# Kernel optimization log

Measured on AMD Instinct MI355X. Metric: run time of the kernel, lower is better.

## Reference

```python
import jax, jax.numpy as jnp
import numpy as np

B, D, L, E, R = 16384, 512, 3, 4, 128

def setup_inputs() -> dict:
    key = jax.random.key(0)
    ks = jax.random.split(key, 6)
    scale = 0.05  # keep tanh in its non-saturated regime, like glorot-ish init
    return {
        "x":  jax.random.normal(ks[0], (B, D), dtype=jnp.float32),
        "Us": jax.random.normal(ks[1], (L, E, D, R), dtype=jnp.float32) * scale,
        "Cs": jax.random.normal(ks[2], (L, E, R, R), dtype=jnp.float32) * scale,
        "Vs": jax.random.normal(ks[3], (L, E, D, R), dtype=jnp.float32) * scale,
        "G":  jax.random.normal(ks[4], (L, E, D), dtype=jnp.float32) * scale,
        "b":  jnp.zeros((L, D), dtype=jnp.float32),
    }

def reference(x, Us, Cs, Vs, G, b):
    # x: (B, D). Original keeps x as (B, D, 1); we drop the trailing singleton.
    x0 = x
    xl = x
    num_layers = Us.shape[0]
    for i in range(num_layers):  # small fixed layer count
        U, C, V, g, bias = Us[i], Cs[i], Vs[i], G[i], b[i]
        # per-expert low-rank bilinear transform, fused over experts via einsum
        xv = jnp.tanh(jnp.einsum('edr,bd->ber', V, xl))       # (B, E, R)
        xc = jnp.tanh(jnp.einsum('ers,bes->ber', C, xv))      # (B, E, R)
        xu = jnp.einsum('edr,ber->bed', U, xc)                # (B, E, D)
        cross = x0[:, None, :] * (xu + bias[None, None, :])   # (B, E, D) experts
        # gating: Dense(1, no bias) per expert -> scores (B, E, 1)
        scores = jnp.einsum('bd,ed->be', xl, g)[..., None]
        # NOTE: original applies softmax over the LAST axis of (B, E, 1),
        # a singleton axis, so gates are all ones. Reproduced faithfully.
        gate = jax.nn.softmax(scores, axis=-1)                # (B, E, 1) of ones
        moe = jnp.einsum('bed,be->bd', cross, gate[..., 0])   # (B, D)
        xl = moe + xl
    return xl
```

## Files before the change

### kernel.cpp

```cpp
#include <hip/hip_runtime.h>
#include <hip/hip_bf16.h>

#define BATCH  16384
#define DIM    512
#define NLAYER 3
#define NEXP   4
#define RANK   128

typedef __bf16 bf16_t;
typedef bf16_t bf16x8 __attribute__((ext_vector_type(8)));
typedef bf16_t bf16x4 __attribute__((ext_vector_type(4)));
typedef float  f32x4  __attribute__((ext_vector_type(4)));

__device__ __forceinline__ float tanh_fast(float x) {
    float e = __expf(2.0f * x);
    return 1.0f - 2.0f * __builtin_amdgcn_rcpf(e + 1.0f);
}
__device__ __forceinline__ int swz(int row, int b) { return b ^ ((row & 7) << 4); }

__device__ __forceinline__ bf16x8 ldsr(const bf16_t* base, int row, int kb) {
    return *(const bf16x8*)((const char*)base + row * 1024 + swz(row, kb));
}
__device__ __forceinline__ void ldsw2(bf16_t* base, int row, int cb, bf16_t v) {
    *(bf16_t*)((char*)base + row * 1024 + swz(row, cb)) = v;
}
__device__ __forceinline__ void barrier_lds() {
    asm volatile("s_waitcnt lgkmcnt(0)" ::: "memory");
    __builtin_amdgcn_s_barrier();
}

__global__ void prep_pack(const float* __restrict__ Vs,
                          const float* __restrict__ Us,
                          const float* __restrict__ Cs,
                          bf16_t* __restrict__ Vp,
                          bf16_t* __restrict__ Up,
                          bf16_t* __restrict__ Cp) {
    int t = blockIdx.x * 256 + threadIdx.x;
    if (t < 98304) {
        int lane = t & 63, ni = (t >> 6) & 3, ks = (t >> 8) & 15,
            wn = (t >> 12) & 7, l = t >> 15;
        int c = wn * 64 + ni * 16 + (lane & 15), e = c >> 7, r = c & 127;
        int d0 = ks * 32 + (lane >> 4) * 8;
        const float* src = Vs + ((size_t)(l * NEXP + e) * DIM + d0) * RANK + r;
        bf16x8 v;
        #pragma unroll
        for (int j = 0; j < 8; ++j) v[j] = (bf16_t)src[j * RANK];
        *(bf16x8*)(Vp + (size_t)t * 8) = v;
    } else if (t < 196608) {
        int q = t - 98304;
        int lane = q & 63, ni = (q >> 6) & 3, ks = (q >> 8) & 15,
            wn = (q >> 12) & 7, l = q >> 15;
        int d = wn * 64 + ni * 16 + (lane & 15);
        int k0 = ks * 32 + (lane >> 4) * 8, e = k0 >> 7, r0 = k0 & 127;
        const float* src = Us + ((size_t)(l * NEXP + e) * DIM + d) * RANK + r0;
        bf16x8 v;
        #pragma unroll
        for (int j = 0; j < 8; ++j) v[j] = (bf16_t)src[j];
        *(bf16x8*)(Up + (size_t)q * 8) = v;
    } else if (t < 221184) {
        int q = t - 196608;
        int lane = q & 63, ni = (q >> 6) & 3, k4 = (q >> 8) & 3,
            wn = (q >> 10) & 7, l = q >> 13;
        int e = wn >> 1, rp = (wn & 1) * 64 + ni * 16 + (lane & 15);
        int s0 = k4 * 32 + (lane >> 4) * 8;
        const float* src = Cs + ((size_t)(l * NEXP + e) * RANK + rp) * RANK + s0;
        bf16x8 v;
        #pragma unroll
        for (int j = 0; j < 8; ++j) v[j] = (bf16_t)src[j];
        *(bf16x8*)(Cp + (size_t)q * 8) = v;
    }
}


__global__ __launch_bounds__(512)
void fused3(const float* __restrict__ x,
            const bf16_t* __restrict__ Vp,
            const bf16_t* __restrict__ Up,
            const bf16_t* __restrict__ Cp,
            const float* __restrict__ bb,
            float* __restrict__ out)
{
    __shared__ __align__(16) char smem[65536];
    bf16_t* bufA = (bf16_t*)smem;
    bf16_t* bufB = (bf16_t*)(smem + 32768);

    const int tid  = threadIdx.x;
    const int lane = tid & 63;
    const int wn   = tid >> 6;
    const int lr   = lane & 15;
    const int lg   = lane >> 4;
    const int m0   = blockIdx.x * 32;

    #pragma unroll
    for (int it = 0; it < 8; ++it) {
        int q = tid + 512 * it;
        int row = q >> 7, c4 = (q & 127) << 2;
        float4 v = *(const float4*)(x + (size_t)(m0 + row) * DIM + c4);
        bf16x4 b4 = { (bf16_t)v.x, (bf16_t)v.y, (bf16_t)v.z, (bf16_t)v.w };
        *(bf16x4*)((char*)bufA + row * 1024 + swz(row, c4 * 2)) = b4;
    }
    f32x4  xlf[2][4];
    bf16x4 x0r[2][4];
    #pragma unroll
    for (int mi = 0; mi < 2; ++mi)
        #pragma unroll
        for (int ni = 0; ni < 4; ++ni)
            #pragma unroll
            for (int j = 0; j < 4; ++j) {
                int row = mi * 16 + lg * 4 + j, col = wn * 64 + ni * 16 + lr;
                float v = x[(size_t)(m0 + row) * DIM + col];
                xlf[mi][ni][j] = v;
                x0r[mi][ni][j] = (bf16_t)v;
            }
    barrier_lds();

    #pragma unroll 1
    for (int l = 0; l < NLAYER; ++l) {
        bf16_t* xl_b = (l & 1) ? bufB : bufA;
        bf16_t* xv_b = (l & 1) ? bufA : bufB;

        const bf16_t* Vw = Vp + (((size_t)l * 8 + wn) << 15) + lane * 8;
        const bf16_t* Uw = Up + (((size_t)l * 8 + wn) << 15) + lane * 8;
        const bf16_t* Cw = Cp + (((size_t)l * 8 + wn) << 13) + lane * 8;

        {
            f32x4 a1[2][4] = {};
            const bf16_t* vp = Vw;
            #pragma unroll 8
            for (int ks = 0; ks < 16; ++ks) {
                bf16x8 bv[4];
                #pragma unroll
                for (int ni = 0; ni < 4; ++ni)
                    bv[ni] = *(const bf16x8*)(vp + ni * 512);
                vp += 2048;
                #pragma unroll
                for (int mi = 0; mi < 2; ++mi) {
                    bf16x8 av = ldsr(xl_b, mi * 16 + lr, ks * 64 + lg * 16);
                    #pragma unroll
                    for (int ni = 0; ni < 4; ++ni)
                        a1[mi][ni] = __builtin_amdgcn_mfma_f32_16x16x32_bf16(
                            av, bv[ni], a1[mi][ni], 0, 0, 0);
                }
            }
            #pragma unroll
            for (int mi = 0; mi < 2; ++mi)
                #pragma unroll
                for (int ni = 0; ni < 4; ++ni)
                    #pragma unroll
                    for (int j = 0; j < 4; ++j)
                        ldsw2(xv_b, mi * 16 + lg * 4 + j,
                              (wn * 64 + ni * 16 + lr) * 2,
                              (bf16_t)tanh_fast(a1[mi][ni][j]));
            barrier_lds();
        }

        {
            const int eb = (wn >> 1) * 256;
            f32x4 a2[2][4] = {};
            #pragma unroll
            for (int k4 = 0; k4 < 4; ++k4) {
                bf16x8 av[2];
                #pragma unroll
                for (int mi = 0; mi < 2; ++mi)
                    av[mi] = ldsr(xv_b, mi * 16 + lr, eb + k4 * 64 + lg * 16);
                #pragma unroll
                for (int ni = 0; ni < 4; ++ni) {
                    bf16x8 bv = *(const bf16x8*)(Cw + (k4 * 4 + ni) * 512);
                    #pragma unroll
                    for (int mi = 0; mi < 2; ++mi)
                        a2[mi][ni] = __builtin_amdgcn_mfma_f32_16x16x32_bf16(
                            av[mi], bv, a2[mi][ni], 0, 0, 0);
                }
            }
            #pragma unroll
            for (int mi = 0; mi < 2; ++mi)
                #pragma unroll
                for (int ni = 0; ni < 4; ++ni)
                    #pragma unroll
                    for (int j = 0; j < 4; ++j)
                        ldsw2(xl_b, mi * 16 + lg * 4 + j,
                              (wn * 64 + ni * 16 + lr) * 2,
                              (bf16_t)tanh_fast(a2[mi][ni][j]));
            barrier_lds();
        }

        {
            f32x4 a3[2][4] = {};
            const bf16_t* up = Uw;
            #pragma unroll 8
            for (int ks = 0; ks < 16; ++ks) {
                bf16x8 bv[4];
                #pragma unroll
                for (int ni = 0; ni < 4; ++ni)
                    bv[ni] = *(const bf16x8*)(up + ni * 512);
                up += 2048;
                #pragma unroll
                for (int mi = 0; mi < 2; ++mi) {
                    bf16x8 av = ldsr(xl_b, mi * 16 + lr, ks * 64 + lg * 16);
                    #pragma unroll
                    for (int ni = 0; ni < 4; ++ni)
                        a3[mi][ni] = __builtin_amdgcn_mfma_f32_16x16x32_bf16(
                            av, bv[ni], a3[mi][ni], 0, 0, 0);
                }
            }

            const float* bl = bb + l * DIM;
            #pragma unroll
            for (int ni = 0; ni < 4; ++ni) {
                int col = wn * 64 + ni * 16 + lr;
                float b4v = 4.0f * bl[col];
                #pragma unroll
                for (int mi = 0; mi < 2; ++mi)
                    #pragma unroll
                    for (int j = 0; j < 4; ++j)
                        xlf[mi][ni][j] +=
                            (float)x0r[mi][ni][j] * (a3[mi][ni][j] + b4v);
            }
        }

        if (l < NLAYER - 1) {
            #pragma unroll
            for (int mi = 0; mi < 2; ++mi)
                #pragma unroll
                for (int ni = 0; ni < 4; ++ni)
                    #pragma unroll
                    for (int j = 0; j < 4; ++j)
                        ldsw2(xv_b, mi * 16 + lg * 4 + j,
                              (wn * 64 + ni * 16 + lr) * 2,
                              (bf16_t)xlf[mi][ni][j]);
            barrier_lds();
        }
    }

    #pragma unroll
    for (int mi = 0; mi < 2; ++mi)
        #pragma unroll
        for (int ni = 0; ni < 4; ++ni)
            #pragma unroll
            for (int j = 0; j < 4; ++j) {
                int row = mi * 16 + lg * 4 + j, col = wn * 64 + ni * 16 + lr;
                out[(size_t)(m0 + row) * DIM + col] = xlf[mi][ni][j];
            }
}


extern "C" void kernel_launch(void* const* d_in, const int* in_sizes, int n_in,
                              void* d_out, int out_size, void* d_ws, size_t ws_size,
                              hipStream_t stream) {
    const float* x  = (const float*)d_in[0];
    const float* Us = (const float*)d_in[1];
    const float* Cs = (const float*)d_in[2];
    const float* Vs = (const float*)d_in[3];
    const float* bb = (const float*)d_in[5];
    float* out = (float*)d_out;

    bf16_t* Vp = (bf16_t*)d_ws;
    bf16_t* Up = Vp + 786432;
    bf16_t* Cp = Up + 786432;

    prep_pack<<<864, 256, 0, stream>>>(Vs, Us, Cs, Vp, Up, Cp);
    fused3<<<BATCH / 32, 512, 0, stream>>>(x, Vp, Up, Cp, bb, out);
}
```

Baseline: 123.4 us.

## Double batch rows per block and park residual state in AGPRs

Each block now handles 64 batch rows instead of 32, so every weight fragment loaded from global memory is reused across four 16-row MFMA tiles rather than two, halving weight traffic per row. The running fp32 residual is kept in accumulation registers through inline accvgpr read/write, freeing VGPRs for the larger accumulator tiles. The residual update is fused with the LDS write-back and the final output store. LDS use doubles to 128 KB, which allows one block per CU, and loop unrolling drops from 8 to 2 to limit register pressure, at some cost in latency hiding.

```diff
diff --git a/kernel.cpp b/kernel.cpp
--- a/kernel.cpp
+++ b/kernel.cpp
@@ -27,6 +27,14 @@
 __device__ __forceinline__ void barrier_lds() {
     asm volatile("s_waitcnt lgkmcnt(0)" ::: "memory");
     __builtin_amdgcn_s_barrier();
+}
+__device__ __forceinline__ void ag_w(float& a, float v) {
+    asm volatile("v_accvgpr_write_b32 %0, %1" : "=a"(a) : "v"(v));
+}
+__device__ __forceinline__ float ag_r(float a) {
+    float v;
+    asm volatile("v_accvgpr_read_b32 %0, %1" : "=v"(v) : "a"(a));
+    return v;
 }
 
 __global__ void prep_pack(const float* __restrict__ Vs,
@@ -80,36 +88,36 @@
             const float* __restrict__ bb,
             float* __restrict__ out)
 {
-    __shared__ __align__(16) char smem[65536];
+    __shared__ __align__(16) char smem[131072];
     bf16_t* bufA = (bf16_t*)smem;
-    bf16_t* bufB = (bf16_t*)(smem + 32768);
+    bf16_t* bufB = (bf16_t*)(smem + 65536);
 
     const int tid  = threadIdx.x;
     const int lane = tid & 63;
     const int wn   = tid >> 6;
     const int lr   = lane & 15;
     const int lg   = lane >> 4;
-    const int m0   = blockIdx.x * 32;
+    const int m0   = blockIdx.x * 64;
 
     #pragma unroll
-    for (int it = 0; it < 8; ++it) {
+    for (int it = 0; it < 16; ++it) {
         int q = tid + 512 * it;
         int row = q >> 7, c4 = (q & 127) << 2;
         float4 v = *(const float4*)(x + (size_t)(m0 + row) * DIM + c4);
         bf16x4 b4 = { (bf16_t)v.x, (bf16_t)v.y, (bf16_t)v.z, (bf16_t)v.w };
         *(bf16x4*)((char*)bufA + row * 1024 + swz(row, c4 * 2)) = b4;
     }
-    f32x4  xlf[2][4];
-    bf16x4 x0r[2][4];
+    float   xs[4][4][4];
+    bf16x4  x0r[4][4];
     #pragma unroll
-    for (int mi = 0; mi < 2; ++mi)
+    for (int mi = 0; mi < 4; ++mi)
         #pragma unroll
         for (int ni = 0; ni < 4; ++ni)
             #pragma unroll
             for (int j = 0; j < 4; ++j) {
                 int row = mi * 16 + lg * 4 + j, col = wn * 64 + ni * 16 + lr;
                 float v = x[(size_t)(m0 + row) * DIM + col];
-                xlf[mi][ni][j] = v;
+                ag_w(xs[mi][ni][j], v);
                 x0r[mi][ni][j] = (bf16_t)v;
             }
     barrier_lds();
@@ -124,9 +132,9 @@
         const bf16_t* Cw = Cp + (((size_t)l * 8 + wn) << 13) + lane * 8;
 
         {
-            f32x4 a1[2][4] = {};
+            f32x4 a1[4][4] = {};
             const bf16_t* vp = Vw;
-            #pragma unroll 8
+            #pragma unroll 2
             for (int ks = 0; ks < 16; ++ks) {
                 bf16x8 bv[4];
                 #pragma unroll
@@ -134,7 +142,7 @@
                     bv[ni] = *(const bf16x8*)(vp + ni * 512);
                 vp += 2048;
                 #pragma unroll
-                for (int mi = 0; mi < 2; ++mi) {
+                for (int mi = 0; mi < 4; ++mi) {
                     bf16x8 av = ldsr(xl_b, mi * 16 + lr, ks * 64 + lg * 16);
                     #pragma unroll
                     for (int ni = 0; ni < 4; ++ni)
@@ -143,7 +151,7 @@
                 }
             }
             #pragma unroll
-            for (int mi = 0; mi < 2; ++mi)
+            for (int mi = 0; mi < 4; ++mi)
                 #pragma unroll
                 for (int ni = 0; ni < 4; ++ni)
                     #pragma unroll
@@ -156,24 +164,24 @@
 
         {
             const int eb = (wn >> 1) * 256;
-            f32x4 a2[2][4] = {};
-            #pragma unroll
+            f32x4 a2[4][4] = {};
+            #pragma unroll 2
             for (int k4 = 0; k4 < 4; ++k4) {
-                bf16x8 av[2];
-                #pragma unroll
-                for (int mi = 0; mi < 2; ++mi)
-                    av[mi] = ldsr(xv_b, mi * 16 + lr, eb + k4 * 64 + lg * 16);
-                #pragma unroll
-                for (int ni = 0; ni < 4; ++ni) {
-                    bf16x8 bv = *(const bf16x8*)(Cw + (k4 * 4 + ni) * 512);
-                    #pragma unroll
-                    for (int mi = 0; mi < 2; ++mi)
+                bf16x8 bv[4];
+                #pragma unroll
+                for (int ni = 0; ni < 4; ++ni)
+                    bv[ni] = *(const bf16x8*)(Cw + (k4 * 4 + ni) * 512);
+                #pragma unroll
+                for (int mi = 0; mi < 4; ++mi) {
+                    bf16x8 av = ldsr(xv_b, mi * 16 + lr, eb + k4 * 64 + lg * 16);
+                    #pragma unroll
+                    for (int ni = 0; ni < 4; ++ni)
                         a2[mi][ni] = __builtin_amdgcn_mfma_f32_16x16x32_bf16(
-                            av[mi], bv, a2[mi][ni], 0, 0, 0);
+                            av, bv[ni], a2[mi][ni], 0, 0, 0);
                 }
             }
             #pragma unroll
-            for (int mi = 0; mi < 2; ++mi)
+            for (int mi = 0; mi < 4; ++mi)
                 #pragma unroll
                 for (int ni = 0; ni < 4; ++ni)
                     #pragma unroll
@@ -185,9 +193,9 @@
         }
 
         {
-            f32x4 a3[2][4] = {};
+            f32x4 a3[4][4] = {};
             const bf16_t* up = Uw;
-            #pragma unroll 8
+            #pragma unroll 2
             for (int ks = 0; ks < 16; ++ks) {
                 bf16x8 bv[4];
                 #pragma unroll
@@ -195,7 +203,7 @@
                     bv[ni] = *(const bf16x8*)(up + ni * 512);
                 up += 2048;
                 #pragma unroll
-                for (int mi = 0; mi < 2; ++mi) {
+                for (int mi = 0; mi < 4; ++mi) {
                     bf16x8 av = ldsr(xl_b, mi * 16 + lr, ks * 64 + lg * 16);
                     #pragma unroll
                     for (int ni = 0; ni < 4; ++ni)
@@ -205,42 +213,31 @@
             }
 
             const float* bl = bb + l * DIM;
+            const bool last = (l == NLAYER - 1);
             #pragma unroll
             for (int ni = 0; ni < 4; ++ni) {
                 int col = wn * 64 + ni * 16 + lr;
                 float b4v = 4.0f * bl[col];
                 #pragma unroll
-                for (int mi = 0; mi < 2; ++mi)
-                    #pragma unroll
-                    for (int j = 0; j < 4; ++j)
-                        xlf[mi][ni][j] +=
-                            (float)x0r[mi][ni][j] * (a3[mi][ni][j] + b4v);
+                for (int mi = 0; mi < 4; ++mi)
+                    #pragma unroll
+                    for (int j = 0; j < 4; ++j) {
+                        float v = ag_r(xs[mi][ni][j]) +
+                                  (float)x0r[mi][ni][j] * (a3[mi][ni][j] + b4v);
+                        if (last) {
+                            int row = mi * 16 + lg * 4 + j;
+                            out[(size_t)(m0 + row) * DIM + col] = v;
+                        } else {
+                            ag_w(xs[mi][ni][j], v);
+                            ldsw2(xv_b, mi * 16 + lg * 4 + j, col * 2, (bf16_t)v);
+                        }
+                    }
             }
         }
 
-        if (l < NLAYER - 1) {
-            #pragma unroll
-            for (int mi = 0; mi < 2; ++mi)
-                #pragma unroll
-                for (int ni = 0; ni < 4; ++ni)
-                    #pragma unroll
-                    for (int j = 0; j < 4; ++j)
-                        ldsw2(xv_b, mi * 16 + lg * 4 + j,
-                              (wn * 64 + ni * 16 + lr) * 2,
-                              (bf16_t)xlf[mi][ni][j]);
+        if (l < NLAYER - 1)
             barrier_lds();
-        }
     }
-
-    #pragma unroll
-    for (int mi = 0; mi < 2; ++mi)
-        #pragma unroll
-        for (int ni = 0; ni < 4; ++ni)
-            #pragma unroll
-            for (int j = 0; j < 4; ++j) {
-                int row = mi * 16 + lg * 4 + j, col = wn * 64 + ni * 16 + lr;
-                out[(size_t)(m0 + row) * DIM + col] = xlf[mi][ni][j];
-            }
 }
 
 
@@ -259,5 +256,5 @@
     bf16_t* Cp = Up + 786432;
 
     prep_pack<<<864, 256, 0, stream>>>(Vs, Us, Cs, Vp, Up, Cp);
-    fused3<<<BATCH / 32, 512, 0, stream>>>(x, Vp, Up, Cp, bb, out);
-}
+    fused3<<<BATCH / 64, 512, 0, stream>>>(x, Vp, Up, Cp, bb, out);
+}
```

Result: slower. 240.6 us (+95.0%).

## Split fused three-layer kernel into one launch per layer

Applied to the files above, without the earlier changes.

Replaces the single kernel that kept xl and x0 in registers across all three layers with a per-layer kernel launched three times. Each launch reads xl and x0 from global memory and writes xl to global, which drops the persistent register state and may lower register pressure or raise occupancy. The cost is extra global traffic, two more kernel launches, and in-place read/write of out on later layers. The unroll factor on the K loops also drops from 8 to 4, and the C-stage loop now loads all four weight vectors before the MFMAs.

```diff
diff --git a/kernel.cpp b/kernel.cpp
--- a/kernel.cpp
+++ b/kernel.cpp
@@ -73,12 +73,13 @@
 
 
 __global__ __launch_bounds__(512)
-void fused3(const float* __restrict__ x,
-            const bf16_t* __restrict__ Vp,
-            const bf16_t* __restrict__ Up,
-            const bf16_t* __restrict__ Cp,
-            const float* __restrict__ bb,
-            float* __restrict__ out)
+void k_layer(const float* xl_in,
+             const float* __restrict__ x0,
+             const bf16_t* __restrict__ Vw0,
+             const bf16_t* __restrict__ Uw0,
+             const bf16_t* __restrict__ Cw0,
+             const float* __restrict__ bl,
+             float* xl_out)
 {
     __shared__ __align__(16) char smem[65536];
     bf16_t* bufA = (bf16_t*)smem;
@@ -95,152 +96,110 @@
     for (int it = 0; it < 8; ++it) {
         int q = tid + 512 * it;
         int row = q >> 7, c4 = (q & 127) << 2;
-        float4 v = *(const float4*)(x + (size_t)(m0 + row) * DIM + c4);
+        float4 v = *(const float4*)(xl_in + (size_t)(m0 + row) * DIM + c4);
         bf16x4 b4 = { (bf16_t)v.x, (bf16_t)v.y, (bf16_t)v.z, (bf16_t)v.w };
         *(bf16x4*)((char*)bufA + row * 1024 + swz(row, c4 * 2)) = b4;
     }
-    f32x4  xlf[2][4];
-    bf16x4 x0r[2][4];
-    #pragma unroll
-    for (int mi = 0; mi < 2; ++mi)
-        #pragma unroll
-        for (int ni = 0; ni < 4; ++ni)
-            #pragma unroll
-            for (int j = 0; j < 4; ++j) {
-                int row = mi * 16 + lg * 4 + j, col = wn * 64 + ni * 16 + lr;
-                float v = x[(size_t)(m0 + row) * DIM + col];
-                xlf[mi][ni][j] = v;
-                x0r[mi][ni][j] = (bf16_t)v;
+    barrier_lds();
+
+    const bf16_t* Vw = Vw0 + ((size_t)wn << 15) + lane * 8;
+    const bf16_t* Uw = Uw0 + ((size_t)wn << 15) + lane * 8;
+    const bf16_t* Cw = Cw0 + ((size_t)wn << 13) + lane * 8;
+
+    {
+        f32x4 a1[2][4] = {};
+        const bf16_t* vp = Vw;
+        #pragma unroll 4
+        for (int ks = 0; ks < 16; ++ks) {
+            bf16x8 bv[4];
+            #pragma unroll
+            for (int ni = 0; ni < 4; ++ni)
+                bv[ni] = *(const bf16x8*)(vp + ni * 512);
+            vp += 2048;
+            #pragma unroll
+            for (int mi = 0; mi < 2; ++mi) {
+                bf16x8 av = ldsr(bufA, mi * 16 + lr, ks * 64 + lg * 16);
+                #pragma unroll
+                for (int ni = 0; ni < 4; ++ni)
+                    a1[mi][ni] = __builtin_amdgcn_mfma_f32_16x16x32_bf16(
+                        av, bv[ni], a1[mi][ni], 0, 0, 0);
             }
-    barrier_lds();
-
-    #pragma unroll 1
-    for (int l = 0; l < NLAYER; ++l) {
-        bf16_t* xl_b = (l & 1) ? bufB : bufA;
-        bf16_t* xv_b = (l & 1) ? bufA : bufB;
-
-        const bf16_t* Vw = Vp + (((size_t)l * 8 + wn) << 15) + lane * 8;
-        const bf16_t* Uw = Up + (((size_t)l * 8 + wn) << 15) + lane * 8;
-        const bf16_t* Cw = Cp + (((size_t)l * 8 + wn) << 13) + lane * 8;
-
-        {
-            f32x4 a1[2][4] = {};
-            const bf16_t* vp = Vw;
-            #pragma unroll 8
-            for (int ks = 0; ks < 16; ++ks) {
-                bf16x8 bv[4];
+        }
+        #pragma unroll
+        for (int mi = 0; mi < 2; ++mi)
+            #pragma unroll
+            for (int ni = 0; ni < 4; ++ni)
+                #pragma unroll
+                for (int j = 0; j < 4; ++j)
+                    ldsw2(bufB, mi * 16 + lg * 4 + j,
+                          (wn * 64 + ni * 16 + lr) * 2,
+                          (bf16_t)tanh_fast(a1[mi][ni][j]));
+        barrier_lds();
+    }
+
+    {
+        const int eb = (wn >> 1) * 256;
+        f32x4 a2[2][4] = {};
+        #pragma unroll
+        for (int k4 = 0; k4 < 4; ++k4) {
+            bf16x8 bv[4];
+            #pragma unroll
+            for (int ni = 0; ni < 4; ++ni)
+                bv[ni] = *(const bf16x8*)(Cw + (k4 * 4 + ni) * 512);
+            #pragma unroll
+            for (int mi = 0; mi < 2; ++mi) {
+                bf16x8 av = ldsr(bufB, mi * 16 + lr, eb + k4 * 64 + lg * 16);
                 #pragma unroll
                 for (int ni = 0; ni < 4; ++ni)
-                    bv[ni] = *(const bf16x8*)(vp + ni * 512);
-                vp += 2048;
-                #pragma unroll
-                for (int mi = 0; mi < 2; ++mi) {
-                    bf16x8 av = ldsr(xl_b, mi * 16 + lr, ks * 64 + lg * 16);
-                    #pragma unroll
-                    for (int ni = 0; ni < 4; ++ni)
-                        a1[mi][ni] = __builtin_amdgcn_mfma_f32_16x16x32_bf16(
-                            av, bv[ni], a1[mi][ni], 0, 0, 0);
+                    a2[mi][ni] = __builtin_amdgcn_mfma_f32_16x16x32_bf16(
+                        av, bv[ni], a2[mi][ni], 0, 0, 0);
+            }
+        }
+        #pragma unroll
+        for (int mi = 0; mi < 2; ++mi)
+            #pragma unroll
+            for (int ni = 0; ni < 4; ++ni)
+                #pragma unroll
+                for (int j = 0; j < 4; ++j)
+                    ldsw2(bufA, mi * 16 + lg * 4 + j,
+                          (wn * 64 + ni * 16 + lr) * 2,
+                          (bf16_t)tanh_fast(a2[mi][ni][j]));
+        barrier_lds();
+    }
+
+    {
+        f32x4 a3[2][4] = {};
+        const bf16_t* up = Uw;
+        #pragma unroll 4
+        for (int ks = 0; ks < 16; ++ks) {
+            bf16x8 bv[4];
+            #pragma unroll
+            for (int ni = 0; ni < 4; ++ni)
+                bv[ni] = *(const bf16x8*)(up + ni * 512);
+            up += 2048;
+            #pragma unroll
+            for (int mi = 0; mi < 2; ++mi) {
+                bf16x8 av = ldsr(bufA, mi * 16 + lr, ks * 64 + lg * 16);
+                #pragma unroll
+                for (int ni = 0; ni < 4; ++ni)
+                    a3[mi][ni] = __builtin_amdgcn_mfma_f32_16x16x32_bf16(
+                        av, bv[ni], a3[mi][ni], 0, 0, 0);
+            }
+        }
+
+        #pragma unroll
+        for (int ni = 0; ni < 4; ++ni) {
+            int col = wn * 64 + ni * 16 + lr;
+            float b4v = 4.0f * bl[col];
+            #pragma unroll
+            for (int mi = 0; mi < 2; ++mi)
+                #pragma unroll
+                for (int j = 0; j < 4; ++j) {
+                    size_t idx = (size_t)(m0 + mi * 16 + lg * 4 + j) * DIM + col;
+                    xl_out[idx] = xl_in[idx] + x0[idx] * (a3[mi][ni][j] + b4v);
                 }
-            }
-            #pragma unroll
-            for (int mi = 0; mi < 2; ++mi)
-                #pragma unroll
-                for (int ni = 0; ni < 4; ++ni)
-                    #pragma unroll
-                    for (int j = 0; j < 4; ++j)
-                        ldsw2(xv_b, mi * 16 + lg * 4 + j,
-                              (wn * 64 + ni * 16 + lr) * 2,
-                              (bf16_t)tanh_fast(a1[mi][ni][j]));
-            barrier_lds();
-        }
-
-        {
-            const int eb = (wn >> 1) * 256;
-            f32x4 a2[2][4] = {};
-            #pragma unroll
-            for (int k4 = 0; k4 < 4; ++k4) {
-                bf16x8 av[2];
-                #pragma unroll
-                for (int mi = 0; mi < 2; ++mi)
-                    av[mi] = ldsr(xv_b, mi * 16 + lr, eb + k4 * 64 + lg * 16);
-                #pragma unroll
-                for (int ni = 0; ni < 4; ++ni) {
-                    bf16x8 bv = *(const bf16x8*)(Cw + (k4 * 4 + ni) * 512);
-                    #pragma unroll
-                    for (int mi = 0; mi < 2; ++mi)
-                        a2[mi][ni] = __builtin_amdgcn_mfma_f32_16x16x32_bf16(
-                            av[mi], bv, a2[mi][ni], 0, 0, 0);
-                }
-            }
-            #pragma unroll
-            for (int mi = 0; mi < 2; ++mi)
-                #pragma unroll
-                for (int ni = 0; ni < 4; ++ni)
-                    #pragma unroll
-                    for (int j = 0; j < 4; ++j)
-                        ldsw2(xl_b, mi * 16 + lg * 4 + j,
-                              (wn * 64 + ni * 16 + lr) * 2,
-                              (bf16_t)tanh_fast(a2[mi][ni][j]));
-            barrier_lds();
-        }
-
-        {
-            f32x4 a3[2][4] = {};
-            const bf16_t* up = Uw;
-            #pragma unroll 8
-            for (int ks = 0; ks < 16; ++ks) {
-                bf16x8 bv[4];
-                #pragma unroll
-                for (int ni = 0; ni < 4; ++ni)
-                    bv[ni] = *(const bf16x8*)(up + ni * 512);
-                up += 2048;
-                #pragma unroll
-                for (int mi = 0; mi < 2; ++mi) {
-                    bf16x8 av = ldsr(xl_b, mi * 16 + lr, ks * 64 + lg * 16);
-                    #pragma unroll
-                    for (int ni = 0; ni < 4; ++ni)
-                        a3[mi][ni] = __builtin_amdgcn_mfma_f32_16x16x32_bf16(
-                            av, bv[ni], a3[mi][ni], 0, 0, 0);
-                }
-            }
-
-            const float* bl = bb + l * DIM;
-            #pragma unroll
-            for (int ni = 0; ni < 4; ++ni) {
-                int col = wn * 64 + ni * 16 + lr;
-                float b4v = 4.0f * bl[col];
-                #pragma unroll
-                for (int mi = 0; mi < 2; ++mi)
-                    #pragma unroll
-                    for (int j = 0; j < 4; ++j)
-                        xlf[mi][ni][j] +=
-                            (float)x0r[mi][ni][j] * (a3[mi][ni][j] + b4v);
-            }
-        }
-
-        if (l < NLAYER - 1) {
-            #pragma unroll
-            for (int mi = 0; mi < 2; ++mi)
-                #pragma unroll
-                for (int ni = 0; ni < 4; ++ni)
-                    #pragma unroll
-                    for (int j = 0; j < 4; ++j)
-                        ldsw2(xv_b, mi * 16 + lg * 4 + j,
-                              (wn * 64 + ni * 16 + lr) * 2,
-                              (bf16_t)xlf[mi][ni][j]);
-            barrier_lds();
-        }
-    }
-
-    #pragma unroll
-    for (int mi = 0; mi < 2; ++mi)
-        #pragma unroll
-        for (int ni = 0; ni < 4; ++ni)
-            #pragma unroll
-            for (int j = 0; j < 4; ++j) {
-                int row = mi * 16 + lg * 4 + j, col = wn * 64 + ni * 16 + lr;
-                out[(size_t)(m0 + row) * DIM + col] = xlf[mi][ni][j];
-            }
+        }
+    }
 }
 
 
@@ -259,5 +218,15 @@
     bf16_t* Cp = Up + 786432;
 
     prep_pack<<<864, 256, 0, stream>>>(Vs, Us, Cs, Vp, Up, Cp);
-    fused3<<<BATCH / 32, 512, 0, stream>>>(x, Vp, Up, Cp, bb, out);
-}
+
+    for (int l = 0; l < NLAYER; ++l) {
+        k_layer<<<BATCH / 32, 512, 0, stream>>>(
+            (l == 0) ? x : out,
+            x,
+            Vp + (size_t)l * 262144,
+            Up + (size_t)l * 262144,
+            Cp + (size_t)l * 65536,
+            bb + (size_t)l * DIM,
+            out);
+    }
+}
```

After: 139.9 us. 13.4% more time.
